# Optimization experiments

Hardware: AMD Instinct MI355X
Metric: run time of the kernel (lower is better)

Reference implementation:

```python
import jax, jax.numpy as jnp
import numpy as np

BATCH = 2048
BUCKETS = 100000
DIM = 64

def setup_inputs() -> dict:
    key = jax.random.key(0)
    k1, k2 = jax.random.split(key)
    inputs = jax.random.uniform(k1, (BATCH, BUCKETS), dtype=jnp.float32)
    embeddings = jax.random.normal(k2, (BUCKETS, DIM), dtype=jnp.float32)
    return {"inputs": inputs, "embeddings": embeddings}

def reference(inputs, embeddings):
    # K.dot(inputs, embeddings): [B, buckets] @ [buckets, dim] -> [B, dim]
    out = jnp.matmul(inputs, embeddings)
    # mean=True branch: divide by count of active buckets, zero where empty
    s = jnp.sum(inputs, axis=-1, keepdims=True)  # [B, 1]
    out = jnp.where(s > 0, out / s, jnp.zeros_like(out))
    return out
```

## Files before the change

### kernel.cpp

```cpp
#include <hip/hip_runtime.h>
#include <hip/hip_bf16.h>

#define BATCH 2048
#define KDIM  100000
#define DIM   64
#define NKB   (KDIM / 32)
#define KP    32
#define ROWS_PER_BLOCK 64

typedef __attribute__((ext_vector_type(8))) short  short8;
typedef __attribute__((ext_vector_type(4))) float  f32x4;

__device__ __forceinline__ unsigned short f2bf(float f) {
    union { float f; unsigned int u; } v; v.f = f;
    unsigned int u = v.u;
    u += 0x7FFFu + ((u >> 16) & 1u);
    return (unsigned short)(u >> 16);
}

__global__ __launch_bounds__(256)
void hashemb_pack(const float* __restrict__ emb, unsigned short* __restrict__ pB) {
    const int kb   = blockIdx.x;
    const int t    = threadIdx.x >> 6;
    const int lane = threadIdx.x & 63;
    const int col  = t * 16 + (lane & 15);
    const int krow = kb * 32 + (lane >> 4) * 8;

    short8 w;
    #pragma unroll
    for (int j = 0; j < 8; ++j)
        w[j] = (short)f2bf(emb[(size_t)(krow + j) * DIM + col]);

    *(short8*)&pB[(((size_t)kb * 4 + t) * 64 + lane) * 8] = w;
}

__global__ __launch_bounds__(256, 4)
void hashemb_matmul(const float* __restrict__ inp,
                    const unsigned short* __restrict__ pB,
                    float* __restrict__ out_acc,
                    float* __restrict__ row_sum) {
    const int tid  = threadIdx.x;
    const int lane = tid & 63;
    const int wid  = tid >> 6;
    const int rb   = blockIdx.x;
    const int kp   = blockIdx.y;

    const int rowbase = rb * ROWS_PER_BLOCK + wid * 16;
    const int arow    = rowbase + (lane & 15);
    const int kgrp    = lane >> 4;

    const float* ap = inp + (size_t)arow * KDIM + kgrp * 8;
    const unsigned short* bp = pB + (size_t)lane * 8;

    f32x4 acc[4];
    #pragma unroll
    for (int t = 0; t < 4; ++t) acc[t] = (f32x4)0.0f;
    float lsum = 0.0f;

    auto step = [&](int kb, f32x4& xa, f32x4& xb, int pf) {
        short8 af;
        #pragma unroll
        for (int j = 0; j < 4; ++j) {
            af[j]     = (short)f2bf(xa[j]);
            af[4 + j] = (short)f2bf(xb[j]);
        }
        lsum += xa[0] + xa[1] + xa[2] + xa[3]
              + xb[0] + xb[1] + xb[2] + xb[3];
        xa = *(const f32x4*)(ap + (size_t)pf * 32);
        xb = *(const f32x4*)(ap + (size_t)pf * 32 + 4);
        const unsigned short* b = bp + (size_t)kb * 4 * 512;
        #pragma unroll
        for (int t = 0; t < 4; ++t) {
            const short8 bf = *(const short8*)(b + t * 512);
            acc[t] = __builtin_amdgcn_mfma_f32_16x16x32_bf16(af, bf, acc[t], 0, 0, 0);
        }
    };

    const int kb0 = kp;
    const int kb1c = (kp + KP < NKB) ? kp + KP : kp;
    f32x4 s0a = *(const f32x4*)(ap + (size_t)kb0 * 32);
    f32x4 s0b = *(const f32x4*)(ap + (size_t)kb0 * 32 + 4);
    f32x4 s1a = *(const f32x4*)(ap + (size_t)kb1c * 32);
    f32x4 s1b = *(const f32x4*)(ap + (size_t)kb1c * 32 + 4);

    for (int kb = kp; kb < NKB; kb += 2 * KP) {
        {
            int pf = kb + 2 * KP; if (pf >= NKB) pf = kb;
            step(kb, s0a, s0b, pf);
        }
        const int kbn = kb + KP;
        if (kbn < NKB) {
            int pf = kbn + 2 * KP; if (pf >= NKB) pf = kbn;
            step(kbn, s1a, s1b, pf);
        }
    }

    lsum += __shfl_xor(lsum, 16, 64);
    lsum += __shfl_xor(lsum, 32, 64);
    if (lane < 16) atomicAdd(&row_sum[rowbase + lane], lsum);

    #pragma unroll
    for (int t = 0; t < 4; ++t) {
        const int col = t * 16 + (lane & 15);
        #pragma unroll
        for (int j = 0; j < 4; ++j) {
            const int row = rowbase + kgrp * 4 + j;
            atomicAdd(&out_acc[row * DIM + col], acc[t][j]);
        }
    }
}

__global__ __launch_bounds__(256)
void hashemb_finalize(float* __restrict__ out, const float* __restrict__ row_sum) {
    const int idx = blockIdx.x * blockDim.x + threadIdx.x;
    if (idx < BATCH * DIM) {
        const float s = row_sum[idx >> 6];
        const float o = out[idx];
        out[idx] = (s > 0.0f) ? (o / s) : 0.0f;
    }
}

extern "C" void kernel_launch(void* const* d_in, const int* in_sizes, int n_in,
                              void* d_out, int out_size, void* d_ws, size_t ws_size,
                              hipStream_t stream) {
    const float* inp = (const float*)d_in[0];
    const float* emb = (const float*)d_in[1];
    float* out = (float*)d_out;
    float* rs  = (float*)d_ws;
    unsigned short* pB = (unsigned short*)((char*)d_ws + 8192);

    hipMemsetAsync(out, 0, (size_t)BATCH * DIM * sizeof(float), stream);
    hipMemsetAsync(rs,  0, (size_t)BATCH * sizeof(float), stream);

    hashemb_pack<<<NKB, 256, 0, stream>>>(emb, pB);

    dim3 grid(BATCH / ROWS_PER_BLOCK, KP);
    hashemb_matmul<<<grid, 256, 0, stream>>>(inp, pB, out, rs);

    hashemb_finalize<<<(BATCH * DIM + 255) / 256, 256, 0, stream>>>(out, rs);
}
```

Before: 242.4 us.

## Give each split-K block a contiguous K range with a deeper A prefetch pipeline

Each K-partition block now handles one contiguous range of 32-wide K chunks instead of a stride-KP interleaving. Within that range the loop keeps eight chunks of A in flight in two register sets of four, rather than two. This targets the latency of the streaming fp32 input reads and improves DRAM page and cache-line locality. The cost is many more live registers, which could lower occupancy under launch_bounds(256,4), plus extra guards on the tail chunks.

```diff
diff --git a/kernel.cpp b/kernel.cpp
--- a/kernel.cpp
+++ b/kernel.cpp
@@ -49,50 +49,62 @@
     const int arow    = rowbase + (lane & 15);
     const int kgrp    = lane >> 4;
 
-    const float* ap = inp + (size_t)arow * KDIM + kgrp * 8;
-    const unsigned short* bp = pB + (size_t)lane * 8;
+    const int base = NKB / KP;
+    const int rem  = NKB % KP;
+    const int cnt  = base + (kp < rem ? 1 : 0);
+    const int kb0  = kp * base + (kp < rem ? kp : rem);
+
+    const float* ap = inp + (size_t)arow * KDIM + (size_t)kb0 * 32 + kgrp * 8;
+    const unsigned short* bp = pB + ((size_t)kb0 * 4 * 64 + lane) * 8;
 
     f32x4 acc[4];
     #pragma unroll
     for (int t = 0; t < 4; ++t) acc[t] = (f32x4)0.0f;
     float lsum = 0.0f;
 
-    auto step = [&](int kb, f32x4& xa, f32x4& xb, int pf) {
-        short8 af;
-        #pragma unroll
-        for (int j = 0; j < 4; ++j) {
-            af[j]     = (short)f2bf(xa[j]);
-            af[4 + j] = (short)f2bf(xb[j]);
-        }
-        lsum += xa[0] + xa[1] + xa[2] + xa[3]
-              + xb[0] + xb[1] + xb[2] + xb[3];
-        xa = *(const f32x4*)(ap + (size_t)pf * 32);
-        xb = *(const f32x4*)(ap + (size_t)pf * 32 + 4);
-        const unsigned short* b = bp + (size_t)kb * 4 * 512;
-        #pragma unroll
-        for (int t = 0; t < 4; ++t) {
-            const short8 bf = *(const short8*)(b + t * 512);
-            acc[t] = __builtin_amdgcn_mfma_f32_16x16x32_bf16(af, bf, acc[t], 0, 0, 0);
+    auto loadA = [&](int idx, f32x4& xa, f32x4& xb) {
+        const int c = (idx < cnt) ? idx : cnt - 1;
+        xa = *(const f32x4*)(ap + (size_t)c * 32);
+        xb = *(const f32x4*)(ap + (size_t)c * 32 + 4);
+    };
+
+    auto consume = [&](int idx, f32x4& xa, f32x4& xb) {
+        if (idx < cnt) {
+            short8 af;
+            #pragma unroll
+            for (int j = 0; j < 4; ++j) {
+                af[j]     = (short)f2bf(xa[j]);
+                af[4 + j] = (short)f2bf(xb[j]);
+            }
+            lsum += xa[0] + xa[1] + xa[2] + xa[3]
+                  + xb[0] + xb[1] + xb[2] + xb[3];
+            const unsigned short* b = bp + (size_t)idx * 2048;
+            #pragma unroll
+            for (int t = 0; t < 4; ++t) {
+                const short8 bf = *(const short8*)(b + t * 512);
+                acc[t] = __builtin_amdgcn_mfma_f32_16x16x32_bf16(af, bf, acc[t], 0, 0, 0);
+            }
         }
     };
 
-    const int kb0 = kp;
-    const int kb1c = (kp + KP < NKB) ? kp + KP : kp;
-    f32x4 s0a = *(const f32x4*)(ap + (size_t)kb0 * 32);
-    f32x4 s0b = *(const f32x4*)(ap + (size_t)kb0 * 32 + 4);
-    f32x4 s1a = *(const f32x4*)(ap + (size_t)kb1c * 32);
-    f32x4 s1b = *(const f32x4*)(ap + (size_t)kb1c * 32 + 4);
+    f32x4 a0a, a0b, a1a, a1b, a2a, a2b, a3a, a3b;
+    f32x4 b0a, b0b, b1a, b1b, b2a, b2b, b3a, b3b;
 
-    for (int kb = kp; kb < NKB; kb += 2 * KP) {
-        {
-            int pf = kb + 2 * KP; if (pf >= NKB) pf = kb;
-            step(kb, s0a, s0b, pf);
-        }
-        const int kbn = kb + KP;
-        if (kbn < NKB) {
-            int pf = kbn + 2 * KP; if (pf >= NKB) pf = kbn;
-            step(kbn, s1a, s1b, pf);
-        }
+    loadA(0, a0a, a0b); loadA(1, a1a, a1b);
+    loadA(2, a2a, a2b); loadA(3, a3a, a3b);
+
+    for (int g = 0; g < cnt; g += 8) {
+        loadA(g + 4, b0a, b0b); loadA(g + 5, b1a, b1b);
+        loadA(g + 6, b2a, b2b); loadA(g + 7, b3a, b3b);
+
+        consume(g + 0, a0a, a0b); consume(g + 1, a1a, a1b);
+        consume(g + 2, a2a, a2b); consume(g + 3, a3a, a3b);
+
+        loadA(g + 8,  a0a, a0b); loadA(g + 9,  a1a, a1b);
+        loadA(g + 10, a2a, a2b); loadA(g + 11, a3a, a3b);
+
+        consume(g + 4, b0a, b0b); consume(g + 5, b1a, b1b);
+        consume(g + 6, b2a, b2b); consume(g + 7, b3a, b3b);
     }
 
     lsum += __shfl_xor(lsum, 16, 64);
```

Measured after the change: 240.4 us. About the same (-0.8%).
